# Optimization experiments

Measured on AMD Instinct MI355X. Metric: run time of the kernel, lower is better.

The kernel has to match this reference:

```python
import jax, jax.numpy as jnp
import numpy as np

K = 512      # per-token feature dim (also per-head dim in this module)
H = 8        # heads
B = 2
T = 2048


def setup_inputs() -> dict:
    key = jax.random.key(0)
    ks = jax.random.split(key, 6)
    s = 1.0 / np.sqrt(K)
    x = jax.random.normal(ks[0], (B, T, K), dtype=jnp.float32)
    # torch Linear(k, k*heads, bias=False): y = x @ W with W stored here as [in, out]
    Wq = jax.random.uniform(ks[1], (K, K * H), dtype=jnp.float32, minval=-s, maxval=s)
    Wk = jax.random.uniform(ks[2], (K, K * H), dtype=jnp.float32, minval=-s, maxval=s)
    Wv = jax.random.uniform(ks[3], (K, K * H), dtype=jnp.float32, minval=-s, maxval=s)
    su = 1.0 / np.sqrt(K * H)
    Wu = jax.random.uniform(ks[4], (K * H, K), dtype=jnp.float32, minval=-su, maxval=su)
    bu = jax.random.uniform(ks[5], (K,), dtype=jnp.float32, minval=-su, maxval=su)
    return {"x": x, "Wq": Wq, "Wk": Wk, "Wv": Wv, "Wu": Wu, "bu": bu}


def reference(x, Wq, Wk, Wv, Wu, bu):
    b, t, k = x.shape
    h = H
    # project and split heads: [b, t, h, k] -> [b, h, t, k]
    q = (x @ Wq).reshape(b, t, h, k).transpose(0, 2, 1, 3)
    kk = (x @ Wk).reshape(b, t, h, k).transpose(0, 2, 1, 3)
    v = (x @ Wv).reshape(b, t, h, k).transpose(0, 2, 1, 3)
    scale = k ** (-0.25)  # applied to both q and k, matching source
    dot = jnp.einsum('bhqd,bhkd->bhqk', q * scale, kk * scale)
    attn = jax.nn.softmax(dot, axis=-1)
    out = jnp.einsum('bhqk,bhkd->bhqd', attn, v)          # [b, h, t, k]
    out = out.transpose(0, 2, 1, 3).reshape(b, t, h * k)   # [b, t, h*k]
    return out @ Wu + bu
```

## Files before the change

### kernel.cpp

```cpp
#include <hip/hip_runtime.h>

typedef unsigned short u16;
typedef unsigned short ushort8 __attribute__((ext_vector_type(8)));
typedef unsigned short us4 __attribute__((ext_vector_type(4)));
typedef __bf16 bf16x8 __attribute__((ext_vector_type(8)));
typedef float f32x4 __attribute__((ext_vector_type(4)));

#define DEV static __device__ __forceinline__

DEV u16 f2bf(float f) {
    unsigned int u = __builtin_bit_cast(unsigned int, f);
    u += 0x7FFFu + ((u >> 16) & 1u);
    return (u16)(u >> 16);
}

DEV f32x4 mfma16(ushort8 a, ushort8 b, f32x4 c) {
    return __builtin_amdgcn_mfma_f32_16x16x32_bf16((bf16x8)a, (bf16x8)b, c, 0, 0, 0);
}

DEV void gload_lds16(const void* g, void* l) {
    __builtin_amdgcn_global_load_lds(
        (const __attribute__((address_space(1))) void*)g,
        (__attribute__((address_space(3))) void*)l, 16, 0, 0);
}

__global__ void cvt_kernel(const float* __restrict__ in, u16* __restrict__ out, int n) {
    int i = (blockIdx.x * 256 + threadIdx.x) * 4;
    if (i >= n) return;
    float4 f = *(const float4*)(in + i);
    us4 o;
    o.x = f2bf(f.x); o.y = f2bf(f.y); o.z = f2bf(f.z); o.w = f2bf(f.w);
    *(us4*)(out + i) = o;
}

__global__ void transpose_cvt(const float* __restrict__ in, u16* __restrict__ out, int R, int C) {
    __shared__ u16 tile[64][72];
    int c0 = blockIdx.x << 6, r0 = blockIdx.y << 6;
    int tx = threadIdx.x & 63, ty = threadIdx.x >> 6;
    for (int i = 0; i < 64; i += 4) {
        int r = i + ty;
        tile[r][tx] = f2bf(in[(size_t)(r0 + r) * C + c0 + tx]);
    }
    __syncthreads();
    for (int i = 0; i < 64; i += 4) {
        int r = i + ty;
        out[(size_t)(c0 + r) * R + r0 + tx] = tile[tx][r];
    }
}

__global__ void transpose_bh(const u16* __restrict__ in, u16* __restrict__ out) {
    __shared__ u16 tile[64][72];
    int bh = blockIdx.z;
    int d0 = blockIdx.x << 6, t0 = blockIdx.y << 6;
    int tx = threadIdx.x & 63, ty = threadIdx.x >> 6;
    const u16* src = in + (size_t)bh * 2048 * 512;
    u16* dst = out + (size_t)bh * 512 * 2048;
    for (int i = 0; i < 64; i += 4) {
        int r = i + ty;
        tile[r][tx] = src[(size_t)(t0 + r) * 512 + d0 + tx];
    }
    __syncthreads();
    for (int i = 0; i < 64; i += 4) {
        int r = i + ty;
        dst[(size_t)(d0 + r) * 2048 + t0 + tx] = tile[tx][r];
    }
}

template <int MODE>
__launch_bounds__(256, 2)
__global__ void gemm_bt(const u16* __restrict__ A, const u16* __restrict__ Bt,
                        float scale, const float* __restrict__ bias,
                        void* __restrict__ out, int Kc) {
    __shared__ u16 Asub[128 * 32];
    __shared__ u16 Bsub[128 * 32];
    const int tid = threadIdx.x, lane = tid & 63, wv = tid >> 6;
    const int bm = blockIdx.y << 7, bn = blockIdx.x << 7;
    const int wr = (wv >> 1) << 6, wc = (wv & 1) << 6;
    const int lr = lane & 15, hi = lane >> 4;

    f32x4 acc[4][4] = {};

    int off0 = (wv * 2048 + lane * 16) >> 1;
    int row0 = off0 >> 5, k0e = off0 & 31;
    int off1 = off0 + 512;
    int row1 = off1 >> 5, k1e = off1 & 31;

    const u16* Ag0 = A + (size_t)(bm + row0) * Kc + k0e;
    const u16* Ag1 = A + (size_t)(bm + row1) * Kc + k1e;
    const u16* Bg0 = Bt + (size_t)(bn + row0) * Kc + k0e;
    const u16* Bg1 = Bt + (size_t)(bn + row1) * Kc + k1e;

    for (int kk = 0; kk < Kc; kk += 32) {
        __syncthreads();
        gload_lds16(Ag0 + kk, &Asub[wv * 1024]);
        gload_lds16(Ag1 + kk, &Asub[wv * 1024 + 512]);
        gload_lds16(Bg0 + kk, &Bsub[wv * 1024]);
        gload_lds16(Bg1 + kk, &Bsub[wv * 1024 + 512]);
        __syncthreads();

        ushort8 a[4], b[4];
#pragma unroll
        for (int m = 0; m < 4; ++m)
            a[m] = *(const ushort8*)&Asub[(wr + m * 16 + lr) * 32 + hi * 8];
#pragma unroll
        for (int n = 0; n < 4; ++n)
            b[n] = *(const ushort8*)&Bsub[(wc + n * 16 + lr) * 32 + hi * 8];
#pragma unroll
        for (int m = 0; m < 4; ++m)
#pragma unroll
            for (int n = 0; n < 4; ++n)
                acc[m][n] = mfma16(a[m], b[n], acc[m][n]);
    }

#pragma unroll
    for (int m = 0; m < 4; ++m)
#pragma unroll
        for (int n = 0; n < 4; ++n)
#pragma unroll
            for (int r = 0; r < 4; ++r) {
                int row = bm + wr + m * 16 + hi * 4 + r;
                int col = bn + wc + n * 16 + lr;
                float v = acc[m][n][r] * scale;
                if constexpr (MODE == 0) {
                    size_t dst = ((size_t)((row >> 11) * 8 + (col >> 9)) * 2048 + (row & 2047)) * 512
                                 + (col & 511);
                    ((u16*)out)[dst] = f2bf(v);
                } else {
                    ((float*)out)[(size_t)row * 512 + col] = v + bias[col];
                }
            }
}

__launch_bounds__(512, 2)
__global__ void attn_kernel(const u16* __restrict__ Q, const u16* __restrict__ K,
                            const u16* __restrict__ Vt, u16* __restrict__ O) {
    __shared__ u16 Klds[2][32 * 512];
    __shared__ u16 Plds[2][128 * 40];
    __shared__ __align__(16) float red[2][128];
    __shared__ __align__(16) float lred[128];
    __shared__ int rflag[2][8];

    const int tid = threadIdx.x, lane = tid & 63, wv = tid >> 6;
    const int lr = lane & 15, hi = lane >> 4;
    const int qh = wv >> 2, ds = wv & 3;

    const int flat = blockIdx.x;
    const int nid = (flat & 7) * 32 + (flat >> 3);
    const int bh = nid >> 4;
    const int q0 = (nid & 15) << 7;

    ushort8 qf[16];
    {
        const char* Qg = (const char*)(Q + ((size_t)bh * 2048 + q0 + wv * 16 + lr) * 512) + hi * 16;
#pragma unroll
        for (int ks = 0; ks < 16; ++ks) qf[ks] = *(const ushort8*)(Qg + ks * 64);
    }

    f32x4 acc[4][8] = {};
    float mrun = -1e30f, lrun = 0.f;

    const char* Kg = (const char*)(K + (size_t)bh * 2048 * 512);
    const char* Vg = (const char*)(Vt + (size_t)bh * 512 * 2048);

    auto s_phase = [&](const char* Kb, f32x4& s0, f32x4& s1) {
        s0 = (f32x4){0.f, 0.f, 0.f, 0.f};
        s1 = (f32x4){0.f, 0.f, 0.f, 0.f};
#pragma unroll
        for (int ks = 0; ks < 16; ++ks) {
            int swz = (ks * 64 + hi * 16) ^ ((lr & 7) << 4);
            ushort8 kf0 = *(const ushort8*)(Kb + lr * 1024 + swz);
            ushort8 kf1 = *(const ushort8*)(Kb + (lr + 16) * 1024 + swz);
            s0 = mfma16(kf0, qf[ks], s0);
            s1 = mfma16(kf1, qf[ks], s1);
        }
    };

    auto softmax_store = [&](const f32x4& s0, const f32x4& s1, int pcb) {
        float mx = fmaxf(fmaxf(fmaxf(s0[0], s0[1]), fmaxf(s0[2], s0[3])),
                         fmaxf(fmaxf(s1[0], s1[1]), fmaxf(s1[2], s1[3])));
        mx = fmaxf(mx, __shfl_xor(mx, 16));
        mx = fmaxf(mx, __shfl_xor(mx, 32));
        float a = 1.0f;
        bool upd = false;
        if (mx > mrun + 11.5f) { a = exp2f(mrun - mx); mrun = mx; upd = true; }
        float p[8];
#pragma unroll
        for (int r = 0; r < 4; ++r) {
            p[r]     = exp2f(s0[r] - mrun);
            p[4 + r] = exp2f(s1[r] - mrun);
        }
        float ps = ((p[0] + p[1]) + (p[2] + p[3])) + ((p[4] + p[5]) + (p[6] + p[7]));
        ps += __shfl_xor(ps, 16);
        ps += __shfl_xor(ps, 32);
        lrun = lrun * a + ps;

        const int qr = wv * 16 + lr;
        char* Pb = (char*)&Plds[pcb][0] + qr * 80;
        uint2 w01, w23;
        w01.x = (unsigned)f2bf(p[0]) | ((unsigned)f2bf(p[1]) << 16);
        w01.y = (unsigned)f2bf(p[2]) | ((unsigned)f2bf(p[3]) << 16);
        w23.x = (unsigned)f2bf(p[4]) | ((unsigned)f2bf(p[5]) << 16);
        w23.y = (unsigned)f2bf(p[6]) | ((unsigned)f2bf(p[7]) << 16);
        *(uint2*)(Pb + hi * 8) = w01;
        *(uint2*)(Pb + 32 + hi * 8) = w23;
        if (hi == 0) red[pcb][qr] = a;
        if (lane == 0) rflag[pcb][wv] = __any(upd) ? 1 : 0;
    };

    auto pv_phase = [&](int pcb, int ktv) {
        int anyupd = rflag[pcb][0] | rflag[pcb][1] | rflag[pcb][2] | rflag[pcb][3]
                   | rflag[pcb][4] | rflag[pcb][5] | rflag[pcb][6] | rflag[pcb][7];
        if (anyupd) {
#pragma unroll
            for (int mf = 0; mf < 4; ++mf) {
                f32x4 a4 = *(const f32x4*)&red[pcb][qh * 64 + mf * 16 + hi * 4];
#pragma unroll
                for (int nf = 0; nf < 8; ++nf)
#pragma unroll
                    for (int r = 0; r < 4; ++r) acc[mf][nf][r] *= a4[r];
            }
        }
        ushort8 pf[4];
#pragma unroll
        for (int mf = 0; mf < 4; ++mf)
            pf[mf] = *(const ushort8*)((const char*)&Plds[pcb][0]
                                       + (qh * 64 + mf * 16 + lr) * 80 + hi * 16);
        __builtin_amdgcn_s_setprio(1);
#pragma unroll
        for (int nf = 0; nf < 8; ++nf) {
            int d = ds * 128 + nf * 16 + lr;
            ushort8 vf = *(const ushort8*)(Vg + (size_t)d * 4096 + (size_t)ktv * 2 + hi * 16);
#pragma unroll
            for (int mf = 0; mf < 4; ++mf) acc[mf][nf] = mfma16(pf[mf], vf, acc[mf][nf]);
        }
        __builtin_amdgcn_s_setprio(0);
    };

    auto prefetch_k = [&](int tt) {
        const char* Kgt = Kg + (size_t)tt * 32 * 1024;
#pragma unroll
        for (int r4 = 0; r4 < 4; ++r4) {
            int r = wv * 4 + r4;
            gload_lds16(Kgt + (size_t)r * 1024 + ((lane ^ (r & 7)) << 4),
                        &Klds[tt & 1][(size_t)r * 512]);
        }
    };

    f32x4 s0c, s1c, s0p, s1p;

    prefetch_k(0);
    __syncthreads();

    prefetch_k(1);
    s_phase((const char*)&Klds[0][0], s0c, s1c);
    __syncthreads();

    for (int t = 1; t < 64; ++t) {
        if (t + 1 < 64) prefetch_k(t + 1);

        s0p = s0c; s1p = s1c;
        s_phase((const char*)&Klds[t & 1][0], s0c, s1c);
        softmax_store(s0p, s1p, (t - 1) & 1);

        __syncthreads();

        pv_phase((t - 1) & 1, (t - 1) << 5);
    }

    softmax_store(s0c, s1c, 1);
    __syncthreads();
    pv_phase(1, 63 << 5);

    if (hi == 0) lred[wv * 16 + lr] = lrun;
    __syncthreads();

    const int b = bh >> 3, h = bh & 7;
#pragma unroll
    for (int mf = 0; mf < 4; ++mf) {
        f32x4 lv = *(const f32x4*)&lred[qh * 64 + mf * 16 + hi * 4];
        f32x4 inv;
#pragma unroll
        for (int r = 0; r < 4; ++r) inv[r] = 1.0f / lv[r];
#pragma unroll
        for (int nf = 0; nf < 8; ++nf) {
            int d = ds * 128 + nf * 16 + lr;
#pragma unroll
            for (int r = 0; r < 4; ++r) {
                int t = q0 + qh * 64 + mf * 16 + hi * 4 + r;
                O[((size_t)(b * 2048 + t)) * 4096 + h * 512 + d] = f2bf(acc[mf][nf][r] * inv[r]);
            }
        }
    }
}

extern "C" void kernel_launch(void* const* d_in, const int* in_sizes, int n_in,
                              void* d_out, int out_size, void* d_ws, size_t ws_size,
                              hipStream_t stream) {
    const float* x  = (const float*)d_in[0];
    const float* Wq = (const float*)d_in[1];
    const float* Wk = (const float*)d_in[2];
    const float* Wv = (const float*)d_in[3];
    const float* Wu = (const float*)d_in[4];
    const float* bu = (const float*)d_in[5];

    char* ws = (char*)d_ws;
    const size_t MB = 1ull << 20;
    u16* xb  = (u16*)(ws + 0);
    u16* Wqt = (u16*)(ws + 4 * MB);
    u16* Wkt = (u16*)(ws + 8 * MB);
    u16* Wvt = (u16*)(ws + 12 * MB);
    u16* Wut = (u16*)(ws + 16 * MB);
    u16* Qb  = (u16*)(ws + 20 * MB);
    u16* Kb  = (u16*)(ws + 52 * MB);
    u16* Vb  = (u16*)(ws + 84 * MB);
    u16* Vtb = (u16*)(ws + 116 * MB);
    u16* Ob  = (u16*)(ws + 84 * MB);

    cvt_kernel<<<2048, 256, 0, stream>>>(x, xb, 2 * 2048 * 512);
    transpose_cvt<<<dim3(64, 8), 256, 0, stream>>>(Wq, Wqt, 512, 4096);
    transpose_cvt<<<dim3(64, 8), 256, 0, stream>>>(Wk, Wkt, 512, 4096);
    transpose_cvt<<<dim3(64, 8), 256, 0, stream>>>(Wv, Wvt, 512, 4096);
    transpose_cvt<<<dim3(8, 64), 256, 0, stream>>>(Wu, Wut, 4096, 512);

    const float s2 = 0.06375871593f;
    gemm_bt<0><<<dim3(32, 32), 256, 0, stream>>>(xb, Wqt, s2,   nullptr, Qb, 512);
    gemm_bt<0><<<dim3(32, 32), 256, 0, stream>>>(xb, Wkt, 1.0f, nullptr, Kb, 512);
    gemm_bt<0><<<dim3(32, 32), 256, 0, stream>>>(xb, Wvt, 1.0f, nullptr, Vb, 512);

    transpose_bh<<<dim3(8, 32, 16), 256, 0, stream>>>(Vb, Vtb);

    attn_kernel<<<256, 512, 0, stream>>>(Qb, Kb, Vtb, Ob);

    gemm_bt<1><<<dim3(4, 32), 256, 0, stream>>>(Ob, Wut, 1.0f, bu, d_out, 4096);
}
```

Before: 497.8 us.

## Batch QKV projections and weight transposes, retile output GEMM, hoist V loads

Merges the three weight transpose-convert launches into one z-indexed launch and the three QKV GEMMs into one batched launch that picks the weight slice, output slice and scale from blockIdx.z. The output projection moves to a dedicated 128x64-tile kernel so it launches 256 blocks instead of 128, which should fill more CUs. In the attention PV phase, all eight V fragment global loads are issued up front so their latency overlaps the rescale and P reads. The cost is more live registers in attention and a smaller per-block tile in the final GEMM.

```diff
diff --git a/kernel.cpp b/kernel.cpp
--- a/kernel.cpp
+++ b/kernel.cpp
@@ -48,6 +48,25 @@
     }
 }
 
+__global__ void transpose_cvt3(const float* __restrict__ in0, const float* __restrict__ in1,
+                               const float* __restrict__ in2, u16* __restrict__ outbase) {
+    __shared__ u16 tile[64][72];
+    const float* in = (blockIdx.z == 0) ? in0 : (blockIdx.z == 1) ? in1 : in2;
+    u16* out = outbase + (size_t)blockIdx.z * 2097152;
+    const int R = 512, C = 4096;
+    int c0 = blockIdx.x << 6, r0 = blockIdx.y << 6;
+    int tx = threadIdx.x & 63, ty = threadIdx.x >> 6;
+    for (int i = 0; i < 64; i += 4) {
+        int r = i + ty;
+        tile[r][tx] = f2bf(in[(size_t)(r0 + r) * C + c0 + tx]);
+    }
+    __syncthreads();
+    for (int i = 0; i < 64; i += 4) {
+        int r = i + ty;
+        out[(size_t)(c0 + r) * R + r0 + tx] = tile[tx][r];
+    }
+}
+
 __global__ void transpose_bh(const u16* __restrict__ in, u16* __restrict__ out) {
     __shared__ u16 tile[64][72];
     int bh = blockIdx.z;
@@ -66,13 +85,16 @@
     }
 }
 
-template <int MODE>
-__launch_bounds__(256, 2)
-__global__ void gemm_bt(const u16* __restrict__ A, const u16* __restrict__ Bt,
-                        float scale, const float* __restrict__ bias,
-                        void* __restrict__ out, int Kc) {
+__launch_bounds__(256, 3)
+__global__ void gemm_qkv(const u16* __restrict__ A, const u16* __restrict__ Btbase,
+                         float s2, u16* __restrict__ outbase) {
     __shared__ u16 Asub[128 * 32];
     __shared__ u16 Bsub[128 * 32];
+    const int Kc = 512;
+    const u16* Bt = Btbase + (size_t)blockIdx.z * 2097152;
+    u16* out = outbase + (size_t)blockIdx.z * 16777216;
+    const float scale = (blockIdx.z == 0) ? s2 : 1.0f;
+
     const int tid = threadIdx.x, lane = tid & 63, wv = tid >> 6;
     const int bm = blockIdx.y << 7, bn = blockIdx.x << 7;
     const int wr = (wv >> 1) << 6, wc = (wv & 1) << 6;
@@ -121,13 +143,71 @@
                 int row = bm + wr + m * 16 + hi * 4 + r;
                 int col = bn + wc + n * 16 + lr;
                 float v = acc[m][n][r] * scale;
-                if constexpr (MODE == 0) {
-                    size_t dst = ((size_t)((row >> 11) * 8 + (col >> 9)) * 2048 + (row & 2047)) * 512
-                                 + (col & 511);
-                    ((u16*)out)[dst] = f2bf(v);
-                } else {
-                    ((float*)out)[(size_t)row * 512 + col] = v + bias[col];
-                }
+                size_t dst = ((size_t)((row >> 11) * 8 + (col >> 9)) * 2048 + (row & 2047)) * 512
+                             + (col & 511);
+                out[dst] = f2bf(v);
+            }
+}
+
+__launch_bounds__(256, 3)
+__global__ void gemm_final(const u16* __restrict__ A, const u16* __restrict__ Bt,
+                           const float* __restrict__ bias, float* __restrict__ out, int Kc) {
+    __shared__ u16 Asub[128 * 32];
+    __shared__ u16 Bsub[64 * 32];
+    const int tid = threadIdx.x, lane = tid & 63, wv = tid >> 6;
+    const int bm = blockIdx.y << 7, bn = blockIdx.x << 6;
+    const int wr = (wv >> 1) << 6, wc = (wv & 1) << 5;
+    const int lr = lane & 15, hi = lane >> 4;
+
+    f32x4 acc[4][2] = {};
+
+    const u16* gsrc[3];
+    u16* ldst[3];
+#pragma unroll
+    for (int j = 0; j < 3; ++j) {
+        int g = wv * 3 + j;
+        int off = g * 512 + lane * 8;
+        if (g < 8) {
+            int row = off >> 5, k = off & 31;
+            gsrc[j] = A + (size_t)(bm + row) * Kc + k;
+            ldst[j] = &Asub[g * 512];
+        } else {
+            int off2 = off - 4096;
+            int row = off2 >> 5, k = off2 & 31;
+            gsrc[j] = Bt + (size_t)(bn + row) * Kc + k;
+            ldst[j] = &Bsub[(g - 8) * 512];
+        }
+    }
+
+    for (int kk = 0; kk < Kc; kk += 32) {
+        __syncthreads();
+#pragma unroll
+        for (int j = 0; j < 3; ++j) gload_lds16(gsrc[j] + kk, ldst[j]);
+        __syncthreads();
+
+        ushort8 a[4], b[2];
+#pragma unroll
+        for (int m = 0; m < 4; ++m)
+            a[m] = *(const ushort8*)&Asub[(wr + m * 16 + lr) * 32 + hi * 8];
+#pragma unroll
+        for (int n = 0; n < 2; ++n)
+            b[n] = *(const ushort8*)&Bsub[(wc + n * 16 + lr) * 32 + hi * 8];
+#pragma unroll
+        for (int m = 0; m < 4; ++m)
+#pragma unroll
+            for (int n = 0; n < 2; ++n)
+                acc[m][n] = mfma16(a[m], b[n], acc[m][n]);
+    }
+
+#pragma unroll
+    for (int m = 0; m < 4; ++m)
+#pragma unroll
+        for (int n = 0; n < 2; ++n)
+#pragma unroll
+            for (int r = 0; r < 4; ++r) {
+                int row = bm + wr + m * 16 + hi * 4 + r;
+                int col = bn + wc + n * 16 + lr;
+                out[(size_t)row * 512 + col] = acc[m][n][r] + bias[col];
             }
 }
 
@@ -208,6 +288,12 @@
     };
 
     auto pv_phase = [&](int pcb, int ktv) {
+        ushort8 vf[8];
+#pragma unroll
+        for (int nf = 0; nf < 8; ++nf) {
+            int d = ds * 128 + nf * 16 + lr;
+            vf[nf] = *(const ushort8*)(Vg + (size_t)d * 4096 + (size_t)ktv * 2 + hi * 16);
+        }
         int anyupd = rflag[pcb][0] | rflag[pcb][1] | rflag[pcb][2] | rflag[pcb][3]
                    | rflag[pcb][4] | rflag[pcb][5] | rflag[pcb][6] | rflag[pcb][7];
         if (anyupd) {
@@ -227,12 +313,9 @@
                                        + (qh * 64 + mf * 16 + lr) * 80 + hi * 16);
         __builtin_amdgcn_s_setprio(1);
 #pragma unroll
-        for (int nf = 0; nf < 8; ++nf) {
-            int d = ds * 128 + nf * 16 + lr;
-            ushort8 vf = *(const ushort8*)(Vg + (size_t)d * 4096 + (size_t)ktv * 2 + hi * 16);
-#pragma unroll
-            for (int mf = 0; mf < 4; ++mf) acc[mf][nf] = mfma16(pf[mf], vf, acc[mf][nf]);
-        }
+        for (int nf = 0; nf < 8; ++nf)
+#pragma unroll
+            for (int mf = 0; mf < 4; ++mf) acc[mf][nf] = mfma16(pf[mf], vf[nf], acc[mf][nf]);
         __builtin_amdgcn_s_setprio(0);
     };
 
@@ -307,29 +390,23 @@
     const size_t MB = 1ull << 20;
     u16* xb  = (u16*)(ws + 0);
     u16* Wqt = (u16*)(ws + 4 * MB);
-    u16* Wkt = (u16*)(ws + 8 * MB);
-    u16* Wvt = (u16*)(ws + 12 * MB);
     u16* Wut = (u16*)(ws + 16 * MB);
     u16* Qb  = (u16*)(ws + 20 * MB);
-    u16* Kb  = (u16*)(ws + 52 * MB);
     u16* Vb  = (u16*)(ws + 84 * MB);
     u16* Vtb = (u16*)(ws + 116 * MB);
+    u16* Kb  = (u16*)(ws + 52 * MB);
     u16* Ob  = (u16*)(ws + 84 * MB);
 
     cvt_kernel<<<2048, 256, 0, stream>>>(x, xb, 2 * 2048 * 512);
-    transpose_cvt<<<dim3(64, 8), 256, 0, stream>>>(Wq, Wqt, 512, 4096);
-    transpose_cvt<<<dim3(64, 8), 256, 0, stream>>>(Wk, Wkt, 512, 4096);
-    transpose_cvt<<<dim3(64, 8), 256, 0, stream>>>(Wv, Wvt, 512, 4096);
+    transpose_cvt3<<<dim3(64, 8, 3), 256, 0, stream>>>(Wq, Wk, Wv, Wqt);
     transpose_cvt<<<dim3(8, 64), 256, 0, stream>>>(Wu, Wut, 4096, 512);
 
     const float s2 = 0.06375871593f;
-    gemm_bt<0><<<dim3(32, 32), 256, 0, stream>>>(xb, Wqt, s2,   nullptr, Qb, 512);
-    gemm_bt<0><<<dim3(32, 32), 256, 0, stream>>>(xb, Wkt, 1.0f, nullptr, Kb, 512);
-    gemm_bt<0><<<dim3(32, 32), 256, 0, stream>>>(xb, Wvt, 1.0f, nullptr, Vb, 512);
+    gemm_qkv<<<dim3(32, 32, 3), 256, 0, stream>>>(xb, Wqt, s2, Qb);
 
     transpose_bh<<<dim3(8, 32, 16), 256, 0, stream>>>(Vb, Vtb);
 
     attn_kernel<<<256, 512, 0, stream>>>(Qb, Kb, Vtb, Ob);
 
-    gemm_bt<1><<<dim3(4, 32), 256, 0, stream>>>(Ob, Wut, 1.0f, bu, d_out, 4096);
-}
+    gemm_final<<<dim3(8, 32), 256, 0, stream>>>(Ob, Wut, bu, (float*)d_out, 4096);
+}
```

Result: slower. 529.3 us (+6.3%).
